# Kernel tuning notes

Hardware: AMD Instinct MI355X
Metric: run time of the kernel (lower is better)

The kernel has to match this reference:

```python
import jax, jax.numpy as jnp
import numpy as np
import math


def hs_pe(x, fr, fi):
    # x: [N, c, h, w], c = cp*3; fr/fi: [max_len, cp] real/imag of freqs_cis.
    N, c, h, w = x.shape
    cp = c // 3
    xs = x.reshape(N, cp, 3, h, w)
    a, b, c3 = xs[:, :, 0], xs[:, :, 1], xs[:, :, 2]
    # rotate (a, b) as complex along h axis
    frh = fr[:h].T[None, :, :, None]  # [1, cp, h, 1]
    fih = fi[:h].T[None, :, :, None]
    a2 = a * frh - b * fih
    b2 = a * fih + b * frh
    # rotate (b2, c3) as complex along w axis
    frw = fr[:w].T[None, :, None, :]  # [1, cp, 1, w]
    fiw = fi[:w].T[None, :, None, :]
    b3 = b2 * frw - c3 * fiw
    c32 = b2 * fiw + c3 * frw
    return jnp.stack([a2, b3, c32], axis=2).reshape(N, c, h, w)


def partition(x, ws, dr):
    # OverlapDilatedWindowPartion
    B, C, H, W = x.shape
    Wsz = ws + dr
    st = Wsz // 2
    nh = math.ceil(H / Wsz)
    nw = math.ceil(W / Wsz)
    x = jnp.pad(x, ((0, 0), (0, 0), (0, nh * Wsz - H), (0, nw * Wsz - W)), mode='reflect')
    x = jnp.concatenate([x, jnp.pad(x[:, :, st:, :], ((0, 0), (0, 0), (0, st), (0, 0)), mode='reflect')], axis=0)
    x = jnp.concatenate([x, jnp.pad(x[:, :, :, st:], ((0, 0), (0, 0), (0, 0), (0, st)), mode='reflect')], axis=0)
    gb = x.shape[0]
    # 'gb c (nh h) (nw w) -> (nh nw gb) c h w'
    x = x.reshape(gb, C, nh, Wsz, nw, Wsz).transpose(2, 4, 0, 1, 3, 5).reshape(nh * nw * gb, C, Wsz, Wsz)
    return x[:, :, :ws, :ws]


def reverse(win, ws, dr, B, H, W):
    # OverlapDilatedWindowReverse
    Wsz = ws + dr
    st = Wsz // 2
    nh = math.ceil(H / Wsz)
    nw = math.ceil(W / Wsz)
    bH, bW = nh * Wsz, nw * Wsz
    win = jnp.pad(win, ((0, 0), (0, 0), (0, dr), (0, dr)))
    C = win.shape[1]
    # '(nh nw g b) c h w -> g b c (nh h) (nw w)'
    x = win.reshape(nh, nw, 4, B, C, Wsz, Wsz).transpose(2, 3, 4, 0, 5, 1, 6).reshape(4, B, C, bH, bW)
    x0 = x[0]
    x1 = jnp.pad(x[1], ((0, 0), (0, 0), (st, 0), (0, 0)))[:, :, :bH, :]
    x2 = jnp.pad(x[2], ((0, 0), (0, 0), (0, 0), (st, 0)))[:, :, :, :bW]
    x3 = jnp.pad(x[3], ((0, 0), (0, 0), (st, 0), (st, 0)))[:, :, :bH, :bW]
    return (x0 + x1 + x2 + x3)[:, :, :H, :W]


HEAD_NUM = 8
WINDOW_SIZE = 8
DILATE_RATE = 4


def setup_inputs() -> dict:
    key = jax.random.key(0)
    k1, k2, k3 = jax.random.split(key, 3)
    B, C, H, W = 1, 576, 192, 192
    x = jax.random.normal(k1, (B, C, H, W), dtype=jnp.float32)
    # rotary frequencies on the unit circle: [window_size, d//3, 2] (real, imag)
    theta = jax.random.uniform(k2, (WINDOW_SIZE, C // (3 * HEAD_NUM) // 3), dtype=jnp.float32) * (2 * np.pi)
    freqs_cis = jnp.stack([jnp.cos(theta), jnp.sin(theta)], axis=-1)
    weight = jax.random.uniform(k3, (1, 1, H, W), dtype=jnp.float32, minval=0.5, maxval=1.5)
    return {"x": x, "freqs_cis": freqs_cis, "weight": weight}


def reference(x, freqs_cis, weight):
    B, C, H, W = x.shape
    ws, dr, n = WINDOW_SIZE, DILATE_RATE, HEAD_NUM
    win = partition(x, ws, dr)  # [Nw, C, ws, ws]
    Nw = win.shape[0]
    d = C // (3 * n)
    # '(k n d)' channel split, k outer, d fastest
    qkv = win.reshape(Nw, 3, n, d, ws, ws).transpose(1, 0, 2, 3, 4, 5).reshape(3, Nw * n, d, ws, ws)
    fr, fi = freqs_cis[..., 0], freqs_cis[..., 1]
    q = hs_pe(qkv[0], fr, fi)
    k = hs_pe(qkv[1], fr, fi)
    v = qkv[2]
    def toseq(t):
        return t.reshape(Nw * n, d, ws * ws).transpose(0, 2, 1)  # [Nw*n, L, d]
    q, k, v = toseq(q), toseq(k), toseq(v)
    scale = jnp.sqrt(jnp.asarray(d, q.dtype))
    attn = jax.nn.softmax(jnp.einsum('nld,nmd->nlm', q, k) / scale, axis=-1)
    out = jnp.einsum('nlm,nmd->nld', attn, v)
    # '(Nw n) (h w) d -> Nw (n d) h w'
    out = out.reshape(Nw, n, ws, ws, d).transpose(0, 1, 4, 2, 3).reshape(Nw, n * d, ws, ws)
    out = reverse(out, ws, dr, B, H, W)
    return out / weight
```

## Files before the change

### kernel.cpp

```cpp
#include <hip/hip_runtime.h>

#define HW 36864
#define HDIM 192
#define NUNITS 8192
#define RDW 4608
#define QO 0
#define KO 768
#define VTO 1536
#define PO 0
#define P_BYTES (384ull * HW * 4)

typedef __fp16 h2  __attribute__((ext_vector_type(2)));
typedef __fp16 v8h __attribute__((ext_vector_type(8)));
typedef float  v4f __attribute__((ext_vector_type(4)));

static __device__ __forceinline__ h2 pk2(float a, float b) {
    return __builtin_amdgcn_cvt_pkrtz(a, b);
}
static __device__ __forceinline__ unsigned h2u(h2 x) {
    union { h2 h; unsigned u; } c; c.h = x; return c.u;
}
static __device__ __forceinline__ h2 u2h(unsigned x) {
    union { unsigned u; h2 h; } c; c.u = x; return c.h;
}
static __device__ __forceinline__ v8h as_v8h(uint4 u) {
    union { uint4 u; v8h h; } c; c.u = u; return c.h;
}

__global__ __launch_bounds__(64)
void attn_mfma(const float* __restrict__ x,
               const float* __restrict__ fc,
               const float* __restrict__ wgt,
               float* __restrict__ out,
               unsigned* __restrict__ wsP)
{
    __shared__ unsigned lds[RDW];
    __shared__ float frs[64], fis[64];
    __shared__ unsigned zblk[4];

    const int lane = threadIdx.x;
    const int gid  = blockIdx.x;
    const int head = gid & 7;
    const int wi   = gid >> 3;
    const int g    = wi & 3;
    const int iw   = (wi >> 2) & 15;
    const int ih   = wi >> 6;

    unsigned* uld = lds;

    {
        float2 t = ((const float2*)fc)[lane];
        frs[lane] = t.x; fis[lane] = t.y;
        if (lane < 4) zblk[lane] = 0;
    }
    __syncthreads();

    const int r = lane >> 3, col = lane & 7;
    const int h0 = ih * 12 + r, w0 = iw * 12 + col;
    int in_h = h0 + ((g & 1) ? 6 : 0); if (in_h >= HDIM) in_h = 2 * HDIM - 2 - in_h;
    int in_w = w0 + ((g & 2) ? 6 : 0); if (in_w >= HDIM) in_w = 2 * HDIM - 2 - in_w;

    float q[24], k[24], v[24];
    const bool wrefl = (g & 2) && (iw == 15);
    if (!wrefl) {
        const int ch4  = lane >> 4;
        const int row  = (lane & 15) >> 1;
        const int half = lane & 1;
        int rh = ih * 12 + row + ((g & 1) ? 6 : 0);
        if (rh >= HDIM) rh = 2 * HDIM - 2 - rh;
        const int wb = iw * 12 + ((g & 2) ? 6 : 0);
        const size_t rowoff = (size_t)rh * HDIM + wb + half * 4;
        unsigned* dst0 = &lds[ch4 * 64 + row * 8 + half * 4];
#pragma unroll
        for (int i = 0; i < 18; ++i) {
            const int c72 = i * 4 + ch4;
            const int qkv = c72 / 24, dd = c72 - qkv * 24;
            const float* src = x + (size_t)(qkv * 192 + head * 24 + dd) * HW + rowoff;
            *(uint4*)(dst0 + (size_t)i * 256) = *(const uint4*)src;
        }
        asm volatile("" ::: "memory");
        const float* Rf = (const float*)lds;
#pragma unroll
        for (int dd = 0; dd < 24; ++dd) q[dd] = Rf[dd * 64 + lane];
#pragma unroll
        for (int dd = 0; dd < 24; ++dd) k[dd] = Rf[(24 + dd) * 64 + lane];
#pragma unroll
        for (int dd = 0; dd < 24; ++dd) v[dd] = Rf[(48 + dd) * 64 + lane];
    } else {
        const float* xb = x + (size_t)(head * 24) * HW + in_h * HDIM + in_w;
#pragma unroll
        for (int dd = 0; dd < 24; ++dd) q[dd] = xb[(size_t)dd * HW];
#pragma unroll
        for (int dd = 0; dd < 24; ++dd) k[dd] = xb[(size_t)dd * HW + (size_t)192 * HW];
#pragma unroll
        for (int dd = 0; dd < 24; ++dd) v[dd] = xb[(size_t)dd * HW + (size_t)384 * HW];
    }

#pragma unroll
    for (int p = 0; p < 8; ++p) {
        const float frr = frs[r * 8 + p],   fir = fis[r * 8 + p];
        const float frc = frs[col * 8 + p], fic = fis[col * 8 + p];
        {
            float a = q[3*p], b = q[3*p+1], c3 = q[3*p+2];
            float b2 = a * fir + b * frr;
            q[3*p]   = a * frr - b * fir;
            q[3*p+1] = b2 * frc - c3 * fic;
            q[3*p+2] = b2 * fic + c3 * frc;
        }
        {
            float a = k[3*p], b = k[3*p+1], c3 = k[3*p+2];
            float b2 = a * fir + b * frr;
            k[3*p]   = a * frr - b * fir;
            k[3*p+1] = b2 * frc - c3 * fic;
            k[3*p+2] = b2 * fic + c3 * frc;
        }
    }

    asm volatile("" ::: "memory");
    {
        const float sc = 0.29448903f;
        uint2* qw = (uint2*)&uld[QO + lane * 12];
        uint2* kw = (uint2*)&uld[KO + lane * 12];
#pragma unroll
        for (int j = 0; j < 3; ++j) {
            qw[2*j]   = make_uint2(h2u(pk2(q[8*j]*sc,   q[8*j+1]*sc)),
                                   h2u(pk2(q[8*j+2]*sc, q[8*j+3]*sc)));
            qw[2*j+1] = make_uint2(h2u(pk2(q[8*j+4]*sc, q[8*j+5]*sc)),
                                   h2u(pk2(q[8*j+6]*sc, q[8*j+7]*sc)));
            kw[2*j]   = make_uint2(h2u(pk2(k[8*j],   k[8*j+1])),
                                   h2u(pk2(k[8*j+2], k[8*j+3])));
            kw[2*j+1] = make_uint2(h2u(pk2(k[8*j+4], k[8*j+5])),
                                   h2u(pk2(k[8*j+6], k[8*j+7])));
        }
    }
    {
#pragma unroll
        for (int i = 0; i < 5; ++i) {
            int idx = lane + i * 64;
            if (idx < 288) uld[VTO + 24 * 36 + idx] = 0;
        }
        __fp16* vt = (__fp16*)&uld[VTO];
        vt[24 * 72 + lane] = (__fp16)1.0f;
#pragma unroll
        for (int dd = 0; dd < 24; ++dd) vt[dd * 72 + lane] = (__fp16)v[dd];
    }
    asm volatile("" ::: "memory");

    const int qq = lane >> 4, l15 = lane & 15;
    v8h Qf[4], Kf[4];
#pragma unroll
    for (int t = 0; t < 4; ++t) {
        const unsigned* qa = (qq < 3) ? &uld[QO + (16*t + l15)*12 + 4*qq] : zblk;
        const unsigned* ka = (qq < 3) ? &uld[KO + (16*t + l15)*12 + 4*qq] : zblk;
        Qf[t] = as_v8h(*(const uint4*)qa);
        Kf[t] = as_v8h(*(const uint4*)ka);
    }
    v8h Vf[2][2];
#pragma unroll
    for (int dt = 0; dt < 2; ++dt)
#pragma unroll
        for (int ks = 0; ks < 2; ++ks)
            Vf[dt][ks] = as_v8h(*(const uint4*)&uld[VTO + (16*dt + l15)*36 + 16*ks + 4*qq]);

#pragma unroll
    for (int tn = 0; tn < 4; ++tn) {
#pragma unroll
        for (int tm = 0; tm < 4; ++tm) {
            v4f c = {0.f, 0.f, 0.f, 0.f};
            c = __builtin_amdgcn_mfma_f32_16x16x32_f16(Kf[tn], Qf[tm], c, 0, 0, 0);
            uint2 w = make_uint2(h2u(pk2(__builtin_amdgcn_exp2f(c[0]),
                                         __builtin_amdgcn_exp2f(c[1]))),
                                 h2u(pk2(__builtin_amdgcn_exp2f(c[2]),
                                         __builtin_amdgcn_exp2f(c[3]))));
            *(uint2*)&uld[PO + (16*tm + l15)*36 + 8*tn + 2*qq] = w;
        }
    }

    v4f O[2][4];
#pragma unroll
    for (int dt = 0; dt < 2; ++dt)
#pragma unroll
        for (int lt = 0; lt < 4; ++lt)
            O[dt][lt] = (v4f){0.f, 0.f, 0.f, 0.f};
#pragma unroll
    for (int lt = 0; lt < 4; ++lt) {
#pragma unroll
        for (int ks = 0; ks < 2; ++ks) {
            v8h Pf = as_v8h(*(const uint4*)&uld[PO + (16*lt + l15)*36 + 16*ks + 4*qq]);
            O[0][lt] = __builtin_amdgcn_mfma_f32_16x16x32_f16(Vf[0][ks], Pf, O[0][lt], 0, 0, 0);
            O[1][lt] = __builtin_amdgcn_mfma_f32_16x16x32_f16(Vf[1][ks], Pf, O[1][lt], 0, 0, 0);
        }
    }

    float inv[4];
#pragma unroll
    for (int lt = 0; lt < 4; ++lt)
        inv[lt] = 1.0f / __shfl(O[1][lt][0], 32 + l15, 64);

    if (wsP) {
        unsigned* sm = uld;
        asm volatile("" ::: "memory");
#pragma unroll
        for (int lt = 0; lt < 4; ++lt) {
            const int   l  = 16*lt + l15;
            const float sc = inv[lt];
            sm[l*12 + 2*qq]     = h2u(pk2(O[0][lt][0]*sc, O[0][lt][1]*sc));
            sm[l*12 + 2*qq + 1] = h2u(pk2(O[0][lt][2]*sc, O[0][lt][3]*sc));
            if (qq < 2) {
                sm[l*12 + 8 + 2*qq] = h2u(pk2(O[1][lt][0]*sc, O[1][lt][1]*sc));
                sm[l*12 + 9 + 2*qq] = h2u(pk2(O[1][lt][2]*sc, O[1][lt][3]*sc));
            }
        }
        asm volatile("" ::: "memory");
        const int goffh = (g & 1) ? 6 : 0, goffw = (g & 2) ? 6 : 0;
        const int oh = ih * 12 + (lane >> 3) + goffh;
        const int ow = iw * 12 + (lane & 7)  + goffw;
        if (oh < HDIM && ow < HDIM) {
            uint4* dst = (uint4*)&wsP[((size_t)(g * 8 + head) * HW
                                       + (size_t)oh * HDIM + ow) * 12];
            const uint4* src = (const uint4*)&sm[lane * 12];
            dst[0] = src[0]; dst[1] = src[1]; dst[2] = src[2];
        }
    } else {
#pragma unroll
        for (int lt = 0; lt < 4; ++lt) {
            const int l  = 16*lt + l15;
            const int oh = ih * 12 + (l >> 3) + ((g & 1) ? 6 : 0);
            const int ow = iw * 12 + (l & 7)  + ((g & 2) ? 6 : 0);
            if (oh < HDIM && ow < HDIM) {
                const float sc = inv[lt] / wgt[oh * HDIM + ow];
                float* ob = out + (size_t)(head * 24) * HW + oh * HDIM + ow;
#pragma unroll
                for (int rg = 0; rg < 4; ++rg)
                    atomicAdd(ob + (size_t)(4*qq + rg) * HW, O[0][lt][rg] * sc);
                if (qq < 2) {
#pragma unroll
                    for (int rg = 0; rg < 4; ++rg)
                        atomicAdd(ob + (size_t)(16 + 4*qq + rg) * HW, O[1][lt][rg] * sc);
                }
            }
        }
    }
}

__global__ __launch_bounds__(256)
void merge_out(const unsigned* __restrict__ wsP,
               const float* __restrict__ wgt,
               float* __restrict__ out)
{
    const int idx  = blockIdx.x * 256 + threadIdx.x;
    const int head = idx / HW;
    const int pix  = idx - head * HW;
    const int h    = pix / HDIM;
    const int w    = pix - h * HDIM;

    float acc[24];
#pragma unroll
    for (int d = 0; d < 24; ++d) acc[d] = 0.f;

#pragma unroll
    for (int g = 0; g < 4; ++g) {
        const int hh = h - ((g & 1) ? 6 : 0);
        const int ww = w - ((g & 2) ? 6 : 0);
        if (hh < 0 || ww < 0) continue;
        if (hh % 12 >= 8 || ww % 12 >= 8) continue;
        const uint4* src = (const uint4*)&wsP[((size_t)(g * 8 + head) * HW + pix) * 12];
#pragma unroll
        for (int j = 0; j < 3; ++j) {
            const uint4 u = src[j];
#pragma unroll
            for (int t = 0; t < 4; ++t) {
                const h2 p = u2h(((const unsigned*)&u)[t]);
                acc[8*j + 2*t]     += (float)p[0];
                acc[8*j + 2*t + 1] += (float)p[1];
            }
        }
    }
    const float wv = wgt[pix];
#pragma unroll
    for (int d = 0; d < 24; ++d)
        out[(size_t)(head * 24 + d) * HW + pix] = acc[d] / wv;
}

extern "C" void kernel_launch(void* const* d_in, const int* in_sizes, int n_in,
                              void* d_out, int out_size, void* d_ws, size_t ws_size,
                              hipStream_t stream) {
    const float* x   = (const float*)d_in[0];
    const float* fc  = (const float*)d_in[1];
    const float* wgt = (const float*)d_in[2];
    float* out = (float*)d_out;

    unsigned* wsP = ws_size >= P_BYTES ? (unsigned*)d_ws : nullptr;

    if (!wsP)
        (void)hipMemsetAsync(out, 0, (size_t)out_size * sizeof(float), stream);
    attn_mfma<<<NUNITS, 64, 0, stream>>>(x, fc, wgt, out, wsP);
    if (wsP)
        merge_out<<<8 * HW / 256, 256, 0, stream>>>(wsP, wgt, out);
}
```

Baseline: 174.0 us.

## Halve LDS staging buffer by loading input in two register-held halves

The global-to-LDS staging of the 72 q/k/v channels is split into two halves of 36 channels, both prefetched into registers and written to LDS one after the other, so the shared buffer shrinks from 4608 to 2688 words. The separate zero block is replaced by a zeroed region inside the V-transpose area, and launch bounds now request 3 blocks. The goal is higher occupancy from lower LDS use, at the cost of more live registers (18 uint4 prefetches) that could cause spills or limit waves per SIMD.

```diff
diff --git a/kernel.cpp b/kernel.cpp
--- a/kernel.cpp
+++ b/kernel.cpp
@@ -3,7 +3,6 @@
 #define HW 36864
 #define HDIM 192
 #define NUNITS 8192
-#define RDW 4608
 #define QO 0
 #define KO 768
 #define VTO 1536
@@ -27,16 +26,15 @@
     union { uint4 u; v8h h; } c; c.u = u; return c.h;
 }
 
-__global__ __launch_bounds__(64)
+__global__ __launch_bounds__(64, 3)
 void attn_mfma(const float* __restrict__ x,
                const float* __restrict__ fc,
                const float* __restrict__ wgt,
                float* __restrict__ out,
                unsigned* __restrict__ wsP)
 {
-    __shared__ unsigned lds[RDW];
+    __shared__ unsigned lds[2688];
     __shared__ float frs[64], fis[64];
-    __shared__ unsigned zblk[4];
 
     const int lane = threadIdx.x;
     const int gid  = blockIdx.x;
@@ -51,7 +49,6 @@
     {
         float2 t = ((const float2*)fc)[lane];
         frs[lane] = t.x; fis[lane] = t.y;
-        if (lane < 4) zblk[lane] = 0;
     }
     __syncthreads();
 
@@ -70,22 +67,39 @@
         if (rh >= HDIM) rh = 2 * HDIM - 2 - rh;
         const int wb = iw * 12 + ((g & 2) ? 6 : 0);
         const size_t rowoff = (size_t)rh * HDIM + wb + half * 4;
+
+        uint4 gA[9], gB[9];
+#pragma unroll
+        for (int i = 0; i < 9; ++i) {
+            const int c = i * 4 + ch4;
+            const int qkv = c / 24, dd = c - qkv * 24;
+            gA[i] = *(const uint4*)(x + (size_t)(qkv * 192 + head * 24 + dd) * HW + rowoff);
+        }
+#pragma unroll
+        for (int i = 0; i < 9; ++i) {
+            const int c = 36 + i * 4 + ch4;
+            const int qkv = c / 24, dd = c - qkv * 24;
+            gB[i] = *(const uint4*)(x + (size_t)(qkv * 192 + head * 24 + dd) * HW + rowoff);
+        }
         unsigned* dst0 = &lds[ch4 * 64 + row * 8 + half * 4];
 #pragma unroll
-        for (int i = 0; i < 18; ++i) {
-            const int c72 = i * 4 + ch4;
-            const int qkv = c72 / 24, dd = c72 - qkv * 24;
-            const float* src = x + (size_t)(qkv * 192 + head * 24 + dd) * HW + rowoff;
-            *(uint4*)(dst0 + (size_t)i * 256) = *(const uint4*)src;
-        }
+        for (int i = 0; i < 9; ++i)
+            *(uint4*)(dst0 + (size_t)i * 256) = gA[i];
         asm volatile("" ::: "memory");
         const float* Rf = (const float*)lds;
 #pragma unroll
         for (int dd = 0; dd < 24; ++dd) q[dd] = Rf[dd * 64 + lane];
 #pragma unroll
-        for (int dd = 0; dd < 24; ++dd) k[dd] = Rf[(24 + dd) * 64 + lane];
-#pragma unroll
-        for (int dd = 0; dd < 24; ++dd) v[dd] = Rf[(48 + dd) * 64 + lane];
+        for (int dd = 0; dd < 12; ++dd) k[dd] = Rf[(24 + dd) * 64 + lane];
+        asm volatile("" ::: "memory");
+#pragma unroll
+        for (int i = 0; i < 9; ++i)
+            *(uint4*)(dst0 + (size_t)i * 256) = gB[i];
+        asm volatile("" ::: "memory");
+#pragma unroll
+        for (int dd = 12; dd < 24; ++dd) k[dd] = Rf[(dd - 12) * 64 + lane];
+#pragma unroll
+        for (int dd = 0; dd < 24; ++dd) v[dd] = Rf[(12 + dd) * 64 + lane];
     } else {
         const float* xb = x + (size_t)(head * 24) * HW + in_h * HDIM + in_w;
 #pragma unroll
@@ -147,11 +161,12 @@
     asm volatile("" ::: "memory");
 
     const int qq = lane >> 4, l15 = lane & 15;
+    const unsigned* zsrc = &uld[VTO + 25 * 36];
     v8h Qf[4], Kf[4];
 #pragma unroll
     for (int t = 0; t < 4; ++t) {
-        const unsigned* qa = (qq < 3) ? &uld[QO + (16*t + l15)*12 + 4*qq] : zblk;
-        const unsigned* ka = (qq < 3) ? &uld[KO + (16*t + l15)*12 + 4*qq] : zblk;
+        const unsigned* qa = (qq < 3) ? &uld[QO + (16*t + l15)*12 + 4*qq] : zsrc;
+        const unsigned* ka = (qq < 3) ? &uld[KO + (16*t + l15)*12 + 4*qq] : zsrc;
         Qf[t] = as_v8h(*(const uint4*)qa);
         Kf[t] = as_v8h(*(const uint4*)ka);
     }
```

After: 203.2 us. +16.8%, slower.
